# Kernel tuning notes

Hardware: AMD Instinct MI355X
Metric: run time of the kernel (lower is better)

The kernel has to match this reference:

```python
import jax, jax.numpy as jnp
import numpy as np

B, T, I = 256, 384, 32      # batch, seq_len, input_size
M, D, O = 128, 64, 128      # ring positions, embedding_dim, num_outputs
K = 2                       # attention_radius -> 2K+1 = 5 neighbors
TEMP = 8.0                  # attention_temperature
EPS = 1e-5                  # torch LayerNorm default eps


def setup_inputs() -> dict:
    key = jax.random.key(0)
    ks = jax.random.split(key, 12)
    def lin(kw, kb, fan_in, shape_w, shape_b):
        lim = 1.0 / np.sqrt(fan_in)
        W = jax.random.uniform(kw, shape_w, jnp.float32, -lim, lim)
        b = jax.random.uniform(kb, shape_b, jnp.float32, -lim, lim)
        return W, b
    Wp, bp = lin(ks[0], ks[1], I, (I, D), (D,))
    Wg, bg = lin(ks[2], ks[3], D, (D, 1), (1,))
    Wo, bo = lin(ks[4], ks[5], D, (D, O), (O,))
    return {
        "x": jax.random.normal(ks[6], (B, T, I), jnp.float32),
        "ptr_init": jax.random.uniform(ks[7], (B,), jnp.float32) * M,
        "Wp": Wp, "bp": bp,
        "gamma": jnp.ones((D,), jnp.float32),
        "beta": jnp.zeros((D,), jnp.float32),
        "jump_dest": jax.random.uniform(ks[8], (M,), jnp.float32) * M,
        "Wg": Wg, "bg": bg,
        "ctx_strength": jnp.asarray(0.2, jnp.float32),
        "Wo": Wo, "bo": bo,
    }


def reference(x, ptr_init, Wp, bp, gamma, beta, jump_dest, Wg, bg, ctx_strength, Wo, bo):
    offsets = jnp.arange(-K, K + 1)               # [2K+1]
    bidx = jnp.arange(B)[:, None]                 # [B,1] batch index for gather/scatter
    half = M / 2.0
    ctx_scale = jax.nn.sigmoid(ctx_strength)

    def step(carry, x_t):
        ring, hidden, ptr = carry                 # [B,M,D], [B,D], [B]
        emb = jnp.tanh(x_t @ Wp + bp)             # input projection + activation
        # Gaussian attention over circular neighborhood of floor(ptr)
        base = jnp.clip(jnp.floor(ptr).astype(jnp.int32), 0, M - 1)
        idx = (base[:, None] + offsets[None, :]) % M            # [B,2K+1]
        delta = jnp.mod(idx.astype(ptr.dtype) - ptr[:, None] + half, M) - half
        w = jax.nn.softmax(-(delta ** 2) / TEMP, axis=1)        # [B,2K+1]
        neigh = ring[bidx, idx]                                  # gather [B,2K+1,D]
        ctx = jnp.sum(w[:, :, None] * neigh, axis=1)             # [B,D]
        state = jnp.tanh(emb + ctx_scale * ctx + hidden)
        # LayerNorm (biased variance, affine)
        mu = jnp.mean(state, axis=-1, keepdims=True)
        var = jnp.var(state, axis=-1, keepdims=True)
        hidden_new = (state - mu) * jax.lax.rsqrt(var + EPS) * gamma + beta
        # scatter-add weighted state back into the ring
        ring = ring.at[bidx, idx].add(w[:, :, None] * state[:, None, :])
        # pointer update: hard STE gate between learned jump and +1 walk
        cur = jnp.clip(ptr.astype(jnp.int32), 0, M - 1)
        jump_target = jump_dest[cur]
        jl = (state @ Wg + bg)[:, 0]
        probs = jax.nn.sigmoid(jl)
        gate = (probs > 0.5).astype(state.dtype) - jax.lax.stop_gradient(probs) + probs
        walk = (ptr + 1.0) % M
        ptr_new = jnp.where(gate > 0.5, jump_target, walk)
        return (ring, hidden_new, ptr_new), None

    ring0 = jnp.zeros((B, M, D), x.dtype)
    h0 = jnp.zeros((B, D), x.dtype)
    (ring, hidden, ptr), _ = jax.lax.scan(step, (ring0, h0, ptr_init), jnp.swapaxes(x, 0, 1))
    logits = hidden @ Wo + bo                     # [B, O]
    return logits
```

## Files before the change

kernel.cpp:

```cpp
#include <hip/hip_runtime.h>
#include <hip/hip_bf16.h>


#define BB 256
#define TT 384
#define II 32
#define MM 128
#define DD 64
#define OO 128
#define CH 8
#define CHF (CH * II)
#define NC (TT / CH)
#define K2 0.1803368801f
#define PR 132

typedef float v2f __attribute__((ext_vector_type(2)));

__device__ __forceinline__ float bfbits(unsigned int lo16) {
    return __uint_as_float(lo16 << 16);
}
__device__ __forceinline__ float ldf(const void* p, long long i, bool isbf) {
    if (isbf) return bfbits((unsigned int)((const unsigned short*)p)[i]);
    return ((const float*)p)[i];
}

template <int CTRL>
__device__ __forceinline__ float dpp_add(float x) {
    int s = __builtin_amdgcn_update_dpp(0, __float_as_int(x), CTRL, 0xf, 0xf, true);
    return x + __int_as_float(s);
}
__device__ __forceinline__ void reduce3(float& a, float& b, float& c) {
    a = dpp_add<0x111>(a); b = dpp_add<0x111>(b); c = dpp_add<0x111>(c);
    a = dpp_add<0x112>(a); b = dpp_add<0x112>(b); c = dpp_add<0x112>(c);
    a = dpp_add<0x114>(a); b = dpp_add<0x114>(b); c = dpp_add<0x114>(c);
    a = dpp_add<0x118>(a); b = dpp_add<0x118>(b); c = dpp_add<0x118>(c);
    a = dpp_add<0x142>(a); b = dpp_add<0x142>(b); c = dpp_add<0x142>(c);
    a = dpp_add<0x143>(a); b = dpp_add<0x143>(b); c = dpp_add<0x143>(c);
    a = __int_as_float(__builtin_amdgcn_readlane(__float_as_int(a), 63));
    b = __int_as_float(__builtin_amdgcn_readlane(__float_as_int(b), 63));
    c = __int_as_float(__builtin_amdgcn_readlane(__float_as_int(c), 63));
}

__device__ __forceinline__ float fast_tanh(float x) {
    float e = __builtin_amdgcn_exp2f(x * 2.885390082f);
    return fmaf(-2.0f, __builtin_amdgcn_rcpf(e + 1.0f), 1.0f);
}

#define P1R 128
__global__ __launch_bounds__(256, 1)
void emb_kernel(const void* __restrict__ x, const void* __restrict__ Wp,
                const void* __restrict__ bp, const void* __restrict__ gamma,
                const void* __restrict__ jump_dest,
                float* __restrict__ embw, float* __restrict__ tabw)
{
    __shared__ float xw[P1R * II];
    __shared__ float wps[II * DD];
    __shared__ float bps[DD];
    const int tid = threadIdx.x;
    const bool isbf = (((const unsigned int*)gamma)[0] == 0x3f803f80u);

    if (blockIdx.x == 0 && tid < MM) {
        const float jd = ldf(jump_dest, tid, isbf);
        int bj = (int)jd; bj = min(bj, MM - 1);
        const float fj = jd - (float)bj;
        float e[5], se = 0.0f;
        #pragma unroll
        for (int j = 0; j < 5; j++) {
            const float d = (float)(j - 2) - fj;
            e[j] = __builtin_amdgcn_exp2f(d * d * -K2);
            se += e[j];
        }
        const float inv = __builtin_amdgcn_rcpf(se);
        #pragma unroll
        for (int j = 0; j < 5; j++) tabw[tid * 8 + j] = e[j] * inv;
        tabw[tid * 8 + 5] = __int_as_float(bj);
        tabw[tid * 8 + 6] = 0.0f; tabw[tid * 8 + 7] = 0.0f;
    }

    const long long r0 = (long long)blockIdx.x * P1R;
    for (int i = tid; i < II * DD; i += 256) wps[i] = ldf(Wp, i, isbf);
    if (tid < DD) bps[tid] = ldf(bp, tid, isbf);
    for (int i = tid; i < P1R * II; i += 256) xw[i] = ldf(x, r0 * II + i, isbf);
    __syncthreads();
    const int d = tid & 63, rg = tid >> 6;
    for (int rr = rg; rr < P1R; rr += 4) {
        float acc = bps[d];
        #pragma unroll
        for (int k = 0; k < II; k++) acc = fmaf(xw[rr * II + k], wps[k * DD + d], acc);
        embw[(r0 + rr) * DD + d] = fast_tanh(acc);
    }
}

__global__ __launch_bounds__(64, 1)
void ring_scan_fast(const void* __restrict__ ptr_init,
                    const void* __restrict__ gamma,
                    const void* __restrict__ beta,
                    const void* __restrict__ Wg,
                    const void* __restrict__ bg,
                    const void* __restrict__ cs,
                    const void* __restrict__ Wo,
                    const void* __restrict__ bo,
                    const float* __restrict__ embw,
                    const float* __restrict__ tabg,
                    void* __restrict__ out)
{
    __shared__ float ring[PR * DD];
    __shared__ float hsh[DD];

    const int b = blockIdx.x;
    const int lane = threadIdx.x;
    const bool isbf = (((const unsigned int*)gamma)[0] == 0x3f803f80u);

    {
        float4 z4 = make_float4(0.f, 0.f, 0.f, 0.f);
        #pragma unroll
        for (int i = 0; i < (PR * DD) / (4 * 64); i++)
            ((float4*)ring)[lane + i * 64] = z4;
        ring[(PR * DD) - 256 + lane] = 0.0f;
    }

    const float gam = ldf(gamma, lane, isbf);
    const float bet = ldf(beta, lane, isbf);
    const float wgv = ldf(Wg, lane, isbf);
    const float bgv = ldf(bg, 0, isbf);
    const float csv = 1.0f / (1.0f + expf(-ldf(cs, 0, isbf)));

    const float p0 = ldf(ptr_init, b, isbf);
    int sbase = __builtin_amdgcn_readfirstlane(min(max((int)floorf(p0), 0), MM - 1));
    const float frac = p0 - (float)sbase;
    float w0, w1, w2, w3, w4;
    {
        float e[5], se = 0.0f;
        #pragma unroll
        for (int j = 0; j < 5; j++) {
            const float d = (float)(j - 2) - frac;
            e[j] = __builtin_amdgcn_exp2f(d * d * -K2);
            se += e[j];
        }
        const float inv = __builtin_amdgcn_rcpf(se);
        w0 = e[0] * inv; w1 = e[1] * inv; w2 = e[2] * inv; w3 = e[3] * inv; w4 = e[4] * inv;
    }

    float sn = 0.0f, hid = 0.0f;

    const float* eb = embw + (size_t)b * TT * DD + lane;
    float ec[CH], en[CH];
    #pragma unroll
    for (int k = 0; k < CH; k++) ec[k] = eb[k * DD];

    for (int tc = 0; tc < NC; tc++) {
        const bool more = (tc + 1 < NC);
        if (more) {
            #pragma unroll
            for (int k = 0; k < CH; k++) en[k] = eb[((tc + 1) * CH + k) * DD];
        }

        #pragma unroll
        for (int tt = 0; tt < CH; tt++) {
            const float* ce = tabg + (sbase << 3);
            const float c0 = ce[0], c1 = ce[1], c2 = ce[2], c3 = ce[3], c4 = ce[4];
            const int bjc = __float_as_int(ce[5]);

            float* rb = ring + sbase * DD + lane;
            const float nb0 = rb[0 * DD], nb1 = rb[1 * DD], nb2 = rb[2 * DD],
                        nb3 = rb[3 * DD], nb4 = rb[4 * DD];

            const float ctx = fmaf(w0, nb0, fmaf(w1, nb1, 0.0f)) +
                              fmaf(w2, nb2, fmaf(w3, nb3, w4 * nb4));
            const float snn = fast_tanh(fmaf(csv, ctx, ec[tt] + hid));

            float r0 = snn, r1 = snn * snn, r2 = snn * wgv;
            reduce3(r0, r1, r2);

            const float nv0 = fmaf(w0, snn, nb0), nv1 = fmaf(w1, snn, nb1),
                        nv2 = fmaf(w2, snn, nb2), nv3 = fmaf(w3, snn, nb3),
                        nv4 = fmaf(w4, snn, nb4);
            rb[0 * DD] = nv0; rb[1 * DD] = nv1; rb[2 * DD] = nv2;
            rb[3 * DD] = nv3; rb[4 * DD] = nv4;
            if (sbase <= 3 || sbase >= MM - 4) {
                const float nv[5] = {nv0, nv1, nv2, nv3, nv4};
                #pragma unroll
                for (int j = 0; j < 5; j++) {
                    const int p = sbase + j;
                    if (p < 4)        ring[(p + MM) * DD + lane] = nv[j];
                    else if (p >= MM) ring[(p - MM) * DD + lane] = nv[j];
                }
            }

            const float mu = r0 * (1.0f / 64.0f);
            const float var = fmaf(-mu, mu, r1 * (1.0f / 64.0f));
            const float rstd = __builtin_amdgcn_rsqf(var + 1e-5f);
            hid = fmaf((snn - mu) * rstd, gam, bet);

            const float jl = r2 + bgv;
            const bool jump = __builtin_amdgcn_readfirstlane(__float_as_int(jl)) > 0;
            sbase = __builtin_amdgcn_readfirstlane(jump ? bjc : ((sbase + 1) & (MM - 1)));
            w0 = jump ? c0 : w0; w1 = jump ? c1 : w1; w2 = jump ? c2 : w2;
            w3 = jump ? c3 : w3; w4 = jump ? c4 : w4;
            sn = snn;
        }
        if (more) {
            #pragma unroll
            for (int k = 0; k < CH; k++) ec[k] = en[k];
        }
    }

    hsh[lane] = hid;
    float a0 = ldf(bo, lane, isbf);
    float a1 = ldf(bo, lane + 64, isbf);
    #pragma unroll 8
    for (int d = 0; d < DD; d++) {
        const float h = hsh[d];
        a0 = fmaf(h, ldf(Wo, d * OO + lane, isbf), a0);
        a1 = fmaf(h, ldf(Wo, d * OO + lane + 64, isbf), a1);
    }
    if (isbf) {
        __hip_bfloat16* o = (__hip_bfloat16*)out;
        o[(size_t)b * OO + lane] = __float2bfloat16(a0);
        o[(size_t)b * OO + lane + 64] = __float2bfloat16(a1);
    } else {
        float* o = (float*)out;
        o[(size_t)b * OO + lane] = a0;
        o[(size_t)b * OO + lane + 64] = a1;
    }
}

__device__ __forceinline__ float emb_dot(const float* xrow, const v2f* wp2, float bpv) {
    v2f acc = {0.0f, 0.0f};
    const v2f* xv = (const v2f*)xrow;
    #pragma unroll
    for (int k = 0; k < II / 2; k++)
        acc = __builtin_elementwise_fma(xv[k], wp2[k], acc);
    return acc.x + acc.y + bpv;
}
__device__ __forceinline__ float fast_tanh_s(float x) {
    float ax = fabsf(x);
    float e = __builtin_amdgcn_exp2f(ax * 2.885390082f);
    float r = 1.0f - 2.0f * __builtin_amdgcn_rcpf(e + 1.0f);
    return copysignf(r, x);
}

__global__ __launch_bounds__(64, 1)
void ring_scan_fallback(const void* __restrict__ x,
                        const void* __restrict__ ptr_init,
                        const void* __restrict__ Wp,
                        const void* __restrict__ bp,
                        const void* __restrict__ gamma,
                        const void* __restrict__ beta,
                        const void* __restrict__ jump_dest,
                        const void* __restrict__ Wg,
                        const void* __restrict__ bg,
                        const void* __restrict__ cs,
                        const void* __restrict__ Wo,
                        const void* __restrict__ bo,
                        void* __restrict__ out)
{
    __shared__ float ring[MM * DD];
    __shared__ float xbuf[2][CHF];
    __shared__ float wtab[5 * MM];
    __shared__ float hsh[DD];
    const int b = blockIdx.x;
    const int lane = threadIdx.x;
    const bool isbf = (((const unsigned int*)gamma)[0] == 0x3f803f80u);
    {
        float4 z = make_float4(0.f, 0.f, 0.f, 0.f);
        #pragma unroll
        for (int i = 0; i < (MM * DD) / (4 * 64); i++)
            ((float4*)ring)[lane + i * 64] = z;
    }
    v2f wp2[II / 2];
    #pragma unroll
    for (int k = 0; k < II / 2; k++) {
        wp2[k].x = ldf(Wp, (2 * k) * DD + lane, isbf);
        wp2[k].y = ldf(Wp, (2 * k + 1) * DD + lane, isbf);
    }
    const float bpv = ldf(bp, lane, isbf);
    const float gam = ldf(gamma, lane, isbf);
    const float bet = ldf(beta, lane, isbf);
    const float wgv = ldf(Wg, lane, isbf);
    const float bgv = ldf(bg, 0, isbf);
    const float csv = 1.0f / (1.0f + expf(-ldf(cs, 0, isbf)));
    int bjA, bjB; float fjA, fjB;
    #pragma unroll
    for (int h = 0; h < 2; h++) {
        const int m = lane + h * 64;
        const float jd = ldf(jump_dest, m, isbf);
        int bj = (int)jd; bj = min(bj, MM - 1);
        const float fj = jd - (float)bj;
        float e[5], se = 0.0f;
        #pragma unroll
        for (int j = 0; j < 5; j++) {
            const float d = (float)(j - 2) - fj;
            e[j] = __builtin_amdgcn_exp2f(d * d * -K2);
            se += e[j];
        }
        const float inv = __builtin_amdgcn_rcpf(se);
        #pragma unroll
        for (int j = 0; j < 5; j++) wtab[j * MM + m] = e[j] * inv;
        if (h == 0) { bjA = bj; fjA = fj; } else { bjB = bj; fjB = fj; }
    }
    const float p0 = ldf(ptr_init, b, isbf);
    int base = min(max((int)floorf(p0), 0), MM - 1);
    float frac = p0 - (float)base;
    float w[5];
    {
        float se = 0.0f;
        #pragma unroll
        for (int j = 0; j < 5; j++) {
            const float d = (float)(j - 2) - frac;
            w[j] = __builtin_amdgcn_exp2f(d * d * -K2);
            se += w[j];
        }
        const float inv = __builtin_amdgcn_rcpf(se);
        #pragma unroll
        for (int j = 0; j < 5; j++) w[j] *= inv;
    }
    float pre[5] = {0, 0, 0, 0, 0};
    float patch[5] = {0, 0, 0, 0, 0};
    float state = 0.0f, hidden = 0.0f;
    const float* xf = (const float*)x + (size_t)b * TT * II;
    const unsigned short* xu = (const unsigned short*)x + (size_t)b * TT * II;
    {
        float4 v;
        if (isbf) {
            uint2 q = ((const uint2*)xu)[lane];
            v.x = bfbits(q.x & 0xffffu); v.y = bfbits(q.x >> 16);
            v.z = bfbits(q.y & 0xffffu); v.w = bfbits(q.y >> 16);
        } else v = ((const float4*)xf)[lane];
        ((float4*)xbuf[0])[lane] = v;
    }
    float emb = fast_tanh_s(emb_dot(xbuf[0], wp2, bpv));
    for (int tc = 0; tc < NC; tc++) {
        const float* xc = xbuf[tc & 1];
        const bool more = (tc + 1 < NC);
        float4 nv;
        if (more) {
            if (isbf) {
                uint2 q = ((const uint2*)(xu + (size_t)(tc + 1) * CHF))[lane];
                nv.x = bfbits(q.x & 0xffffu); nv.y = bfbits(q.x >> 16);
                nv.z = bfbits(q.y & 0xffffu); nv.w = bfbits(q.y >> 16);
            } else nv = ((const float4*)(xf + (size_t)(tc + 1) * CHF))[lane];
        }
        #pragma unroll
        for (int tt = 0; tt < CH; tt++) {
            const int bl = __builtin_amdgcn_readlane(bjA, base & 63);
            const int bh = __builtin_amdgcn_readlane(bjB, base & 63);
            const int bj_c = (base < 64) ? bl : bh;
            const int fl = __builtin_amdgcn_readlane(__float_as_int(fjA), base & 63);
            const int fh = __builtin_amdgcn_readlane(__float_as_int(fjB), base & 63);
            const float fj_c = __int_as_float((base < 64) ? fl : fh);
            const int walkrow = (base + 3) & (MM - 1);
            const float preW4 = ring[walkrow * DD + lane];
            float preJ[5], wnJ[5];
            #pragma unroll
            for (int j = 0; j < 5; j++) {
                const int r = (bj_c + j + (MM - 2)) & (MM - 1);
                preJ[j] = ring[r * DD + lane];
                wnJ[j] = wtab[j * MM + base];
            }
            float nb[5], A = 0.0f, Bc = 0.0f;
            #pragma unroll
            for (int j = 0; j < 5; j++) nb[j] = fmaf(patch[j], state, pre[j]);
            #pragma unroll
            for (int j = 0; j < 5; j++) { A = fmaf(w[j], pre[j], A); Bc = fmaf(w[j], patch[j], Bc); }
            const float C = fmaf(csv, A, emb + hidden);
            const float D = csv * Bc;
            const float sn = fast_tanh_s(fmaf(D, state, C));
            #pragma unroll
            for (int j = 0; j < 5; j++) {
                const int r = (base + j + (MM - 2)) & (MM - 1);
                ring[r * DD + lane] = fmaf(w[j], sn, nb[j]);
            }
            float r0 = sn, r1 = sn * sn, r2 = sn * wgv;
            reduce3(r0, r1, r2);
            const float mu = r0 * (1.0f / 64.0f);
            const float var = fmaf(-mu, mu, r1 * (1.0f / 64.0f));
            const float rstd = __builtin_amdgcn_rsqf(var + 1e-5f);
            hidden = fmaf((sn - mu) * rstd, gam, bet);
            const bool jump = (r2 + bgv) > 0.0f;
            const int s = ((bj_c - base + 64) & (MM - 1)) - 64;
            float np[5], nq[5], nw[5];
            np[0] = jump ? preJ[0] : nb[1];  nq[0] = jump ? 0.0f : w[1];
            np[1] = jump ? preJ[1] : nb[2];  nq[1] = jump ? 0.0f : w[2];
            np[2] = jump ? preJ[2] : nb[3];  nq[2] = jump ? 0.0f : w[3];
            np[3] = jump ? preJ[3] : nb[4];  nq[3] = jump ? 0.0f : w[4];
            np[4] = jump ? preJ[4] : preW4;  nq[4] = 0.0f;
            #pragma unroll
            for (int j = 0; j < 5; j++) nw[j] = jump ? wnJ[j] : w[j];
            if (jump && s >= -4 && s <= 4) {
                #pragma unroll
                for (int j = 0; j < 5; j++) {
                    const int k = j + s;
                    float pv = 0.0f;
                    pv = (k == 0) ? w[0] : pv;
                    pv = (k == 1) ? w[1] : pv;
                    pv = (k == 2) ? w[2] : pv;
                    pv = (k == 3) ? w[3] : pv;
                    pv = (k == 4) ? w[4] : pv;
                    nq[j] = pv;
                }
            }
            base = jump ? bj_c : ((base + 1) & (MM - 1));
            frac = jump ? fj_c : frac;
            #pragma unroll
            for (int j = 0; j < 5; j++) { pre[j] = np[j]; patch[j] = nq[j]; w[j] = nw[j]; }
            state = sn;
            if (tt < CH - 1) {
                emb = fast_tanh_s(emb_dot(xc + (tt + 1) * II, wp2, bpv));
            } else if (more) {
                ((float4*)xbuf[(tc & 1) ^ 1])[lane] = nv;
                emb = fast_tanh_s(emb_dot(xbuf[(tc & 1) ^ 1], wp2, bpv));
            }
        }
    }
    hsh[lane] = hidden;
    float a0 = ldf(bo, lane, isbf);
    float a1 = ldf(bo, lane + 64, isbf);
    #pragma unroll 8
    for (int d = 0; d < DD; d++) {
        const float h = hsh[d];
        a0 = fmaf(h, ldf(Wo, d * OO + lane, isbf), a0);
        a1 = fmaf(h, ldf(Wo, d * OO + lane + 64, isbf), a1);
    }
    if (isbf) {
        __hip_bfloat16* o = (__hip_bfloat16*)out;
        o[(size_t)b * OO + lane] = __float2bfloat16(a0);
        o[(size_t)b * OO + lane + 64] = __float2bfloat16(a1);
    } else {
        float* o = (float*)out;
        o[(size_t)b * OO + lane] = a0;
        o[(size_t)b * OO + lane + 64] = a1;
    }
}

extern "C" void kernel_launch(void* const* d_in, const int* in_sizes, int n_in,
                              void* d_out, int out_size, void* d_ws, size_t ws_size,
                              hipStream_t stream) {
    const size_t emb_bytes = (size_t)BB * TT * DD * sizeof(float);
    const size_t need = emb_bytes + MM * 8 * sizeof(float);
    if (ws_size >= need) {
        float* embw = (float*)d_ws;
        float* tabw = (float*)((char*)d_ws + emb_bytes);
        emb_kernel<<<(BB * TT) / P1R, 256, 0, stream>>>(d_in[0], d_in[2], d_in[3],
                                                        d_in[4], d_in[6], embw, tabw);
        ring_scan_fast<<<BB, 64, 0, stream>>>(d_in[1], d_in[4], d_in[5],
                                              d_in[7], d_in[8], d_in[9], d_in[10],
                                              d_in[11], embw, tabw, d_out);
    } else {
        ring_scan_fallback<<<BB, 64, 0, stream>>>(
            d_in[0], d_in[1], d_in[2], d_in[3], d_in[4], d_in[5],
            d_in[6], d_in[7], d_in[8], d_in[9], d_in[10], d_in[11], d_out);
    }
}
```

Measured before the change: 204.6 us.

## Speculatively prefetch next-step ring neighbors and move jump table into LDS

The scan loop now loads both candidate next neighborhoods (walk and jump) right after the scatter write, overlapping them with the cross-lane reduction, and precomputes both candidate contexts so the next step starts with its context ready. The jump-destination weight table moves from global memory into per-block LDS, built by each block, and its next entry is fetched one step ahead. The embedding kernel keeps Wp in registers and uses vectorized x loads. Together these shorten the serial per-step dependency chain, at the cost of extra LDS reads per step and duplicated table setup in every block.

```diff
diff --git a/kernel.cpp b/kernel.cpp
--- a/kernel.cpp
+++ b/kernel.cpp
@@ -46,47 +46,60 @@
     return fmaf(-2.0f, __builtin_amdgcn_rcpf(e + 1.0f), 1.0f);
 }
 
+__device__ __forceinline__ float dot5(float a0, float a1, float a2, float a3, float a4,
+                                      float b0, float b1, float b2, float b3, float b4) {
+    v2f u = {a0, a1}, v = {b0, b1};
+    v2f p = u * v;
+    v2f u2 = {a2, a3}, v2 = {b2, b3};
+    p = __builtin_elementwise_fma(u2, v2, p);
+    return fmaf(a4, b4, p.x + p.y);
+}
+
 #define P1R 128
 __global__ __launch_bounds__(256, 1)
 void emb_kernel(const void* __restrict__ x, const void* __restrict__ Wp,
                 const void* __restrict__ bp, const void* __restrict__ gamma,
-                const void* __restrict__ jump_dest,
-                float* __restrict__ embw, float* __restrict__ tabw)
+                float* __restrict__ embw)
 {
     __shared__ float xw[P1R * II];
-    __shared__ float wps[II * DD];
-    __shared__ float bps[DD];
     const int tid = threadIdx.x;
     const bool isbf = (((const unsigned int*)gamma)[0] == 0x3f803f80u);
-
-    if (blockIdx.x == 0 && tid < MM) {
-        const float jd = ldf(jump_dest, tid, isbf);
-        int bj = (int)jd; bj = min(bj, MM - 1);
-        const float fj = jd - (float)bj;
-        float e[5], se = 0.0f;
-        #pragma unroll
-        for (int j = 0; j < 5; j++) {
-            const float d = (float)(j - 2) - fj;
-            e[j] = __builtin_amdgcn_exp2f(d * d * -K2);
-            se += e[j];
-        }
-        const float inv = __builtin_amdgcn_rcpf(se);
-        #pragma unroll
-        for (int j = 0; j < 5; j++) tabw[tid * 8 + j] = e[j] * inv;
-        tabw[tid * 8 + 5] = __int_as_float(bj);
-        tabw[tid * 8 + 6] = 0.0f; tabw[tid * 8 + 7] = 0.0f;
-    }
-
     const long long r0 = (long long)blockIdx.x * P1R;
-    for (int i = tid; i < II * DD; i += 256) wps[i] = ldf(Wp, i, isbf);
-    if (tid < DD) bps[tid] = ldf(bp, tid, isbf);
-    for (int i = tid; i < P1R * II; i += 256) xw[i] = ldf(x, r0 * II + i, isbf);
+    const int d = tid & 63, rg = tid >> 6;
+
+    if (isbf) {
+        const uint4* xg = (const uint4*)((const unsigned short*)x + r0 * II);
+        for (int i = tid; i < (P1R * II) / 8; i += 256) {
+            uint4 q = xg[i];
+            float4* dst = (float4*)(xw + i * 8);
+            dst[0] = make_float4(bfbits(q.x & 0xffffu), bfbits(q.x >> 16),
+                                 bfbits(q.y & 0xffffu), bfbits(q.y >> 16));
+            dst[1] = make_float4(bfbits(q.z & 0xffffu), bfbits(q.z >> 16),
+                                 bfbits(q.w & 0xffffu), bfbits(q.w >> 16));
+        }
+    } else {
+        const float4* xg = (const float4*)((const float*)x + r0 * II);
+        for (int i = tid; i < (P1R * II) / 4; i += 256)
+            ((float4*)xw)[i] = xg[i];
+    }
+
+    float wp[II];
+    #pragma unroll
+    for (int k = 0; k < II; k++) wp[k] = ldf(Wp, k * DD + d, isbf);
+    const float bpv = ldf(bp, d, isbf);
     __syncthreads();
-    const int d = tid & 63, rg = tid >> 6;
+
     for (int rr = rg; rr < P1R; rr += 4) {
-        float acc = bps[d];
-        #pragma unroll
-        for (int k = 0; k < II; k++) acc = fmaf(xw[rr * II + k], wps[k * DD + d], acc);
+        const float4* xr = (const float4*)(xw + rr * II);
+        float acc = bpv;
+        #pragma unroll
+        for (int k = 0; k < II / 4; k++) {
+            float4 q = xr[k];
+            acc = fmaf(q.x, wp[4 * k + 0], acc);
+            acc = fmaf(q.y, wp[4 * k + 1], acc);
+            acc = fmaf(q.z, wp[4 * k + 2], acc);
+            acc = fmaf(q.w, wp[4 * k + 3], acc);
+        }
         embw[(r0 + rr) * DD + d] = fast_tanh(acc);
     }
 }
@@ -95,16 +108,17 @@
 void ring_scan_fast(const void* __restrict__ ptr_init,
                     const void* __restrict__ gamma,
                     const void* __restrict__ beta,
+                    const void* __restrict__ jump_dest,
                     const void* __restrict__ Wg,
                     const void* __restrict__ bg,
                     const void* __restrict__ cs,
                     const void* __restrict__ Wo,
                     const void* __restrict__ bo,
                     const float* __restrict__ embw,
-                    const float* __restrict__ tabg,
                     void* __restrict__ out)
 {
     __shared__ float ring[PR * DD];
+    __shared__ float tab[MM * 8];
     __shared__ float hsh[DD];
 
     const int b = blockIdx.x;
@@ -116,7 +130,6 @@
         #pragma unroll
         for (int i = 0; i < (PR * DD) / (4 * 64); i++)
             ((float4*)ring)[lane + i * 64] = z4;
-        ring[(PR * DD) - 256 + lane] = 0.0f;
     }
 
     const float gam = ldf(gamma, lane, isbf);
@@ -124,6 +137,25 @@
     const float wgv = ldf(Wg, lane, isbf);
     const float bgv = ldf(bg, 0, isbf);
     const float csv = 1.0f / (1.0f + expf(-ldf(cs, 0, isbf)));
+
+    #pragma unroll
+    for (int h = 0; h < 2; h++) {
+        const int m = lane + h * 64;
+        const float jd = ldf(jump_dest, m, isbf);
+        int bj = (int)jd; bj = min(bj, MM - 1);
+        const float fj = jd - (float)bj;
+        float e[5], se = 0.0f;
+        #pragma unroll
+        for (int j = 0; j < 5; j++) {
+            const float dd = (float)(j - 2) - fj;
+            e[j] = __builtin_amdgcn_exp2f(dd * dd * -K2);
+            se += e[j];
+        }
+        const float inv = __builtin_amdgcn_rcpf(se);
+        #pragma unroll
+        for (int j = 0; j < 5; j++) tab[m * 8 + j] = e[j] * inv;
+        tab[m * 8 + 5] = __int_as_float(bj);
+    }
 
     const float p0 = ldf(ptr_init, b, isbf);
     int sbase = __builtin_amdgcn_readfirstlane(min(max((int)floorf(p0), 0), MM - 1));
@@ -133,15 +165,21 @@
         float e[5], se = 0.0f;
         #pragma unroll
         for (int j = 0; j < 5; j++) {
-            const float d = (float)(j - 2) - frac;
-            e[j] = __builtin_amdgcn_exp2f(d * d * -K2);
+            const float dd = (float)(j - 2) - frac;
+            e[j] = __builtin_amdgcn_exp2f(dd * dd * -K2);
             se += e[j];
         }
         const float inv = __builtin_amdgcn_rcpf(se);
         w0 = e[0] * inv; w1 = e[1] * inv; w2 = e[2] * inv; w3 = e[3] * inv; w4 = e[4] * inv;
     }
 
-    float sn = 0.0f, hid = 0.0f;
+    const float* te = tab + (sbase << 3);
+    float c0 = te[0], c1 = te[1], c2 = te[2], c3 = te[3], c4 = te[4];
+    int bjc = __float_as_int(te[5]);
+
+    float nb0 = 0.f, nb1 = 0.f, nb2 = 0.f, nb3 = 0.f, nb4 = 0.f;
+    float ctxn = 0.0f;
+    float hid = 0.0f;
 
     const float* eb = embw + (size_t)b * TT * DD + lane;
     float ec[CH], en[CH];
@@ -157,28 +195,20 @@
 
         #pragma unroll
         for (int tt = 0; tt < CH; tt++) {
-            const float* ce = tabg + (sbase << 3);
-            const float c0 = ce[0], c1 = ce[1], c2 = ce[2], c3 = ce[3], c4 = ce[4];
-            const int bjc = __float_as_int(ce[5]);
+            const float z = fmaf(csv, ctxn, ec[tt] + hid);
+            const float snn = fast_tanh(z);
 
             float* rb = ring + sbase * DD + lane;
-            const float nb0 = rb[0 * DD], nb1 = rb[1 * DD], nb2 = rb[2 * DD],
-                        nb3 = rb[3 * DD], nb4 = rb[4 * DD];
-
-            const float ctx = fmaf(w0, nb0, fmaf(w1, nb1, 0.0f)) +
-                              fmaf(w2, nb2, fmaf(w3, nb3, w4 * nb4));
-            const float snn = fast_tanh(fmaf(csv, ctx, ec[tt] + hid));
-
-            float r0 = snn, r1 = snn * snn, r2 = snn * wgv;
-            reduce3(r0, r1, r2);
-
-            const float nv0 = fmaf(w0, snn, nb0), nv1 = fmaf(w1, snn, nb1),
-                        nv2 = fmaf(w2, snn, nb2), nv3 = fmaf(w3, snn, nb3),
-                        nv4 = fmaf(w4, snn, nb4);
-            rb[0 * DD] = nv0; rb[1 * DD] = nv1; rb[2 * DD] = nv2;
-            rb[3 * DD] = nv3; rb[4 * DD] = nv4;
+            v2f s2 = {snn, snn};
+            v2f wa = {w0, w1}, na = {nb0, nb1};
+            v2f wbv = {w2, w3}, nbv = {nb2, nb3};
+            v2f nv01 = __builtin_elementwise_fma(wa, s2, na);
+            v2f nv23 = __builtin_elementwise_fma(wbv, s2, nbv);
+            const float nv4 = fmaf(w4, snn, nb4);
+            rb[0 * DD] = nv01.x; rb[1 * DD] = nv01.y; rb[2 * DD] = nv23.x;
+            rb[3 * DD] = nv23.y; rb[4 * DD] = nv4;
             if (sbase <= 3 || sbase >= MM - 4) {
-                const float nv[5] = {nv0, nv1, nv2, nv3, nv4};
+                const float nv[5] = {nv01.x, nv01.y, nv23.x, nv23.y, nv4};
                 #pragma unroll
                 for (int j = 0; j < 5; j++) {
                     const int p = sbase + j;
@@ -187,6 +217,17 @@
                 }
             }
 
+            const int base_w = (sbase + 1) & (MM - 1);
+            const float* rw = ring + base_w * DD + lane;
+            const float* rj = ring + bjc * DD + lane;
+            const float pw0 = rw[0 * DD], pw1 = rw[1 * DD], pw2 = rw[2 * DD],
+                        pw3 = rw[3 * DD], pw4 = rw[4 * DD];
+            const float pj0 = rj[0 * DD], pj1 = rj[1 * DD], pj2 = rj[2 * DD],
+                        pj3 = rj[3 * DD], pj4 = rj[4 * DD];
+
+            float r0 = snn, r1 = snn * snn, r2 = snn * wgv;
+            reduce3(r0, r1, r2);
+
             const float mu = r0 * (1.0f / 64.0f);
             const float var = fmaf(-mu, mu, r1 * (1.0f / 64.0f));
             const float rstd = __builtin_amdgcn_rsqf(var + 1e-5f);
@@ -194,10 +235,20 @@
 
             const float jl = r2 + bgv;
             const bool jump = __builtin_amdgcn_readfirstlane(__float_as_int(jl)) > 0;
-            sbase = __builtin_amdgcn_readfirstlane(jump ? bjc : ((sbase + 1) & (MM - 1)));
+            sbase = __builtin_amdgcn_readfirstlane(jump ? bjc : base_w);
+            const float* t2 = tab + (sbase << 3);
+            const float tc0 = t2[0], tc1 = t2[1], tc2 = t2[2], tc3 = t2[3], tc4 = t2[4];
+            const int tbj = __float_as_int(t2[5]);
+
+            const float ctxW = dot5(w0, w1, w2, w3, w4, pw0, pw1, pw2, pw3, pw4);
+            const float ctxJ = dot5(c0, c1, c2, c3, c4, pj0, pj1, pj2, pj3, pj4);
+
+            ctxn = jump ? ctxJ : ctxW;
+            nb0 = jump ? pj0 : pw0; nb1 = jump ? pj1 : pw1; nb2 = jump ? pj2 : pw2;
+            nb3 = jump ? pj3 : pw3; nb4 = jump ? pj4 : pw4;
             w0 = jump ? c0 : w0; w1 = jump ? c1 : w1; w2 = jump ? c2 : w2;
             w3 = jump ? c3 : w3; w4 = jump ? c4 : w4;
-            sn = snn;
+            c0 = tc0; c1 = tc1; c2 = tc2; c3 = tc3; c4 = tc4; bjc = tbj;
         }
         if (more) {
             #pragma unroll
@@ -436,16 +487,14 @@
 extern "C" void kernel_launch(void* const* d_in, const int* in_sizes, int n_in,
                               void* d_out, int out_size, void* d_ws, size_t ws_size,
                               hipStream_t stream) {
-    const size_t emb_bytes = (size_t)BB * TT * DD * sizeof(float);
-    const size_t need = emb_bytes + MM * 8 * sizeof(float);
+    const size_t need = (size_t)BB * TT * DD * sizeof(float);
     if (ws_size >= need) {
         float* embw = (float*)d_ws;
-        float* tabw = (float*)((char*)d_ws + emb_bytes);
         emb_kernel<<<(BB * TT) / P1R, 256, 0, stream>>>(d_in[0], d_in[2], d_in[3],
-                                                        d_in[4], d_in[6], embw, tabw);
-        ring_scan_fast<<<BB, 64, 0, stream>>>(d_in[1], d_in[4], d_in[5],
+                                                        d_in[4], embw);
+        ring_scan_fast<<<BB, 64, 0, stream>>>(d_in[1], d_in[4], d_in[5], d_in[6],
                                               d_in[7], d_in[8], d_in[9], d_in[10],
-                                              d_in[11], embw, tabw, d_out);
+                                              d_in[11], embw, d_out);
     } else {
         ring_scan_fallback<<<BB, 64, 0, stream>>>(
             d_in[0], d_in[1], d_in[2], d_in[3], d_in[4], d_in[5],
```

Measured after the change: 201.2 us. No clear change (-1.7%).
